# Performance work log

Measured on AMD Instinct MI355X. Metric: run time of the kernel, lower is better.

## Reference

```python
import jax, jax.numpy as jnp
import numpy as np
import math

HEADS = 16
SPH = 64      # size_per_head
KEY = 64      # key_size (defaults to size_per_head)
EMB = 1024
STEP = 3


def extract_seq_patches(x, kernel_size, step):
    # x: [B, L, D] -> [B, L, kernel_size, D]; patch j at pos t is x_pad[t - p_left + j*step]
    B, L, D = x.shape
    k_size = kernel_size + (step - 1) * (kernel_size - 1)
    p_right = (k_size - 1) // 2
    p_left = k_size - 1 - p_right
    xp = jnp.pad(x, ((0, 0), (p_left, p_right), (0, 0)))
    xs = [xp[:, i:i + L] for i in range(0, k_size, step)]  # kernel_size slices
    return jnp.stack(xs, axis=2)


def setup_inputs() -> dict:
    key = jax.random.key(0)
    kx, kq, kk, kv = jax.random.split(key, 4)
    B, L = 2, 4096
    x = jax.random.normal(kx, (B, L, EMB), dtype=jnp.float32)
    W_q = jax.random.normal(kq, (EMB, HEADS * KEY), dtype=jnp.float32) * 0.02
    W_k = jax.random.normal(kk, (EMB, HEADS * KEY), dtype=jnp.float32) * 0.02
    W_v = jax.random.normal(kv, (EMB, HEADS * SPH), dtype=jnp.float32) * 0.02
    return {"x": x, "W_q": W_q, "W_k": W_k, "W_v": W_v}


def _forward(x, W_q, W_k, W_v):
    B, L, D = x.shape
    pad_len = STEP - L % STEP
    x = jnp.pad(x, ((0, 0), (0, pad_len), (0, 0)))
    new_len = L + pad_len
    blocks = new_len // STEP
    q = x @ W_q  # [B, new_len, H*KEY]
    k = x @ W_k
    v = x @ W_v
    ksz = 1 + 2 * (STEP - 1)  # kernel_size = 5
    kp = extract_seq_patches(k, ksz, STEP)  # [B, new_len, ksz, H*KEY]
    vp = extract_seq_patches(v, ksz, STEP)
    # reshape to [B, H, step, blocks, d]
    q = q.reshape(B, blocks, STEP, HEADS, KEY).transpose(0, 3, 2, 1, 4)
    kb = k.reshape(B, blocks, STEP, HEADS, KEY).transpose(0, 3, 2, 1, 4)
    vb = v.reshape(B, blocks, STEP, HEADS, SPH).transpose(0, 3, 2, 1, 4)
    # neighbor patches: [B, H, step, blocks, ksz, d]
    kp = kp.reshape(B, blocks, STEP, ksz, HEADS, KEY).transpose(0, 4, 2, 1, 3, 5)
    vp = vp.reshape(B, blocks, STEP, ksz, HEADS, SPH).transpose(0, 4, 2, 1, 3, 5)
    scale = 1.0 / math.sqrt(KEY)
    # strided attention over blocks (same residue mod step): [B,H,step,blocks,blocks]
    a = jnp.einsum('bhsqk,bhspk->bhsqp', q, kb) * scale
    # block-local neighbor attention: [B,H,step,blocks,ksz]
    ap = jnp.einsum('bhsqk,bhsqnk->bhsqn', q, kp) * scale
    A = jax.nn.softmax(jnp.concatenate([a, ap], axis=-1), axis=-1)
    a, ap = A[..., :blocks], A[..., blocks:]
    o = (jnp.einsum('bhsqp,bhspd->bhsqd', a, vb)
         + jnp.einsum('bhsqn,bhsqnd->bhsqd', ap, vp))
    o = o.transpose(0, 3, 2, 1, 4).reshape(B, new_len, HEADS * SPH)
    return o[:, :L]


def reference(x, W_q, W_k, W_v):
    return _forward(x, W_q, W_k, W_v)
```

## Files before the change

### kernel.cpp

```cpp
#include <hip/hip_runtime.h>
#include <hip/hip_bf16.h>

typedef unsigned int u32;
typedef unsigned short u16;
typedef short s8v __attribute__((ext_vector_type(8)));
typedef short s4v __attribute__((ext_vector_type(4)));
typedef float f4v __attribute__((ext_vector_type(4)));
typedef float f16v __attribute__((ext_vector_type(16)));
typedef u32 u32x2 __attribute__((ext_vector_type(2)));

#define NBLK 1366
#define VROW 1376
#define QSCALE 0.18033688011112042f

__device__ __forceinline__ u16 f2b(float f) {
  u32 u = __builtin_bit_cast(u32, f);
  u = (u + 0x7FFFu + ((u >> 16) & 1u)) >> 16;
  return (u16)u;
}

__device__ __forceinline__ u32 cvtpk(float a, float b) {
  u32 r;
  asm("v_cvt_pk_bf16_f32 %0, %1, %2" : "=v"(r) : "v"(a), "v"(b));
  return r;
}

__device__ __forceinline__ float fexp2(float x) {
#if defined(__has_builtin)
#if __has_builtin(__builtin_amdgcn_exp2f)
  return __builtin_amdgcn_exp2f(x);
#define FEXP2_DONE 1
#endif
#endif
#ifndef FEXP2_DONE
  float r;
  asm("v_exp_f32 %0, %1" : "=v"(r) : "v"(x));
  return r;
#endif
}

__device__ __forceinline__ void gll16(const void* g, void* l) {
  __builtin_amdgcn_global_load_lds(
      (const __attribute__((address_space(1))) u32*)g,
      (__attribute__((address_space(3))) u32*)l, 16, 0, 0);
}

__device__ __forceinline__ f4v mfma32(s8v a, s8v b, f4v c) {
  return __builtin_amdgcn_mfma_f32_16x16x32_bf16(a, b, c, 0, 0, 0);
}

__device__ __forceinline__ f16v mfma3216(s8v a, s8v b, f16v c) {
  return __builtin_amdgcn_mfma_f32_32x32x16_bf16(a, b, c, 0, 0, 0);
}

__device__ __forceinline__ f16v mfma3208(s4v a, s4v b, f16v c) {
#if defined(__has_builtin)
#if __has_builtin(__builtin_amdgcn_mfma_f32_32x32x8bf16_1k)
#define MFMA3208_BUILTIN 1
#endif
#endif
#ifdef MFMA3208_BUILTIN
  return __builtin_amdgcn_mfma_f32_32x32x8bf16_1k(a, b, c, 0, 0, 0);
#else
  f16v d;
  asm("v_mfma_f32_32x32x8_bf16 %0, %1, %2, %3" : "=v"(d) : "v"(a), "v"(b), "v"(c));
  return d;
#endif
}

__device__ __forceinline__ s4v lo4(s8v v) {
  return __builtin_shufflevector(v, v, 0, 1, 2, 3);
}
__device__ __forceinline__ s4v hi4(s8v v) {
  return __builtin_shufflevector(v, v, 4, 5, 6, 7);
}

__global__ __launch_bounds__(256) void k_prep(const float* __restrict__ x,
                                              const float* __restrict__ Wq,
                                              const float* __restrict__ Wk,
                                              const float* __restrict__ Wv,
                                              u16* __restrict__ xb,
                                              u16* __restrict__ Wt,
                                              u16* __restrict__ Vt) {
  const int bid = blockIdx.x;
  const int tid = threadIdx.x;
  if (bid < 4160) {
    long base = ((long)bid * 256 + tid) * 8;
    if (base >= 8320L * 1024L) return;
    int m = (int)(base >> 10);
    int c = (int)(base & 1023);
    int b = m / 4098;
    int t = m - b * 4098;
    s8v pack;
    if (m < 8196 && t < 4096) {
      const float* src = x + ((size_t)b * 4096 + t) * 1024 + c;
      float4 v0 = *(const float4*)(src);
      float4 v1 = *(const float4*)(src + 4);
      pack[0] = (short)f2b(v0.x); pack[1] = (short)f2b(v0.y);
      pack[2] = (short)f2b(v0.z); pack[3] = (short)f2b(v0.w);
      pack[4] = (short)f2b(v1.x); pack[5] = (short)f2b(v1.y);
      pack[6] = (short)f2b(v1.z); pack[7] = (short)f2b(v1.w);
    } else {
#pragma unroll
      for (int i = 0; i < 8; ++i) pack[i] = 0;
    }
    *(s8v*)(xb + base) = pack;
  } else if (bid < 7232) {
    __shared__ float tile[32][33];
    int bid3 = bid - 4160;
    int z = bid3 >> 10;
    int rem = bid3 & 1023;
    const float* W = (z == 0) ? Wq : ((z == 1) ? Wk : Wv);
    u16* dst = Wt + (size_t)z * 1024 * 1024;
    int n0 = (rem & 31) * 32, k0 = (rem >> 5) * 32;
    int tx = tid & 31, ty = tid >> 5;
#pragma unroll
    for (int i = 0; i < 4; ++i)
      tile[ty + i * 8][tx] = W[(size_t)(k0 + ty + i * 8) * 1024 + n0 + tx];
    __syncthreads();
#pragma unroll
    for (int i = 0; i < 4; ++i)
      dst[(size_t)(n0 + ty + i * 8) * 1024 + k0 + tx] = f2b(tile[tx][ty + i * 8]);
  } else {
    int gidx = (bid - 7232) * 256 + tid;
    if (gidx < 6144) {
      u16* dst = Vt + (size_t)gidx * VROW + NBLK;
#pragma unroll
      for (int i = 0; i < 10; ++i) dst[i] = 0;
    } else if (gidx < 6400) {
      Vt[(size_t)6144 * VROW + (gidx - 6144)] = 0;
    }
  }
}

__global__ __launch_bounds__(256) void k_gemm_qkv(const u16* __restrict__ xb,
                                                  const u16* __restrict__ Wt,
                                                  u16* __restrict__ Qp,
                                                  u16* __restrict__ Kp,
                                                  u16* __restrict__ Vt) {
  const int zid = blockIdx.z;
  const int m0 = blockIdx.x * 128;
  const int n0 = blockIdx.y * 128;
  const u16* Bg = Wt + (size_t)zid * 1024 * 1024 + (size_t)n0 * 1024;

  __shared__ __align__(16) u16 shl[16384];
  u16* A0 = shl;
  u16* A1 = shl + 4096;
  u16* B0 = shl + 8192;
  u16* B1 = shl + 12288;

  const int tid = threadIdx.x;
  const int lane = tid & 63;
  const int w = tid >> 6;
  const int wr = w >> 1, wc = w & 1;
  const int lo = lane & 15, g = lane >> 4;

  const int lrow = lane >> 2;
  const int csrc = (lane & 3) ^ ((lane >> 3) & 3);
  const int rsw = (g ^ ((lo >> 1) & 3)) << 4;

  f4v acc[4][4];
#pragma unroll
  for (int i = 0; i < 4; ++i)
#pragma unroll
    for (int j = 0; j < 4; ++j) {
      f4v z = {0.f, 0.f, 0.f, 0.f};
      acc[i][j] = z;
    }

  auto stage = [&](int kt, u16* Ab, u16* Bb) {
#pragma unroll
    for (int c = 0; c < 2; ++c) {
      int rloc = w * 32 + c * 16 + lrow;
      gll16(xb + (size_t)(m0 + rloc) * 1024 + kt + csrc * 8,
            Ab + (w * 32 + c * 16) * 32);
      gll16(Bg + (size_t)rloc * 1024 + kt + csrc * 8,
            Bb + (w * 32 + c * 16) * 32);
    }
  };

  auto compute = [&](const u16* Ab, const u16* Bb) {
    s8v af[4], bf[4];
#pragma unroll
    for (int i = 0; i < 4; ++i) {
      int ar = wr * 64 + i * 16 + lo;
      af[i] = *(const s8v*)((const char*)Ab + ar * 64 + rsw);
      int br = wc * 64 + i * 16 + lo;
      bf[i] = *(const s8v*)((const char*)Bb + br * 64 + rsw);
    }
    __builtin_amdgcn_s_setprio(1);
#pragma unroll
    for (int i = 0; i < 4; ++i)
#pragma unroll
      for (int j = 0; j < 4; ++j)
        acc[i][j] = mfma32(af[i], bf[j], acc[i][j]);
    __builtin_amdgcn_s_setprio(0);
  };

#define BAR_VM4                                             \
  asm volatile("s_waitcnt vmcnt(4)" ::: "memory");          \
  __builtin_amdgcn_s_barrier();                             \
  asm volatile("" ::: "memory");
#define BAR_LGKM                                            \
  asm volatile("s_waitcnt lgkmcnt(0)" ::: "memory");        \
  __builtin_amdgcn_s_barrier();                             \
  asm volatile("" ::: "memory");

  stage(0, A0, B0);
#pragma unroll 1
  for (int kk = 0; kk < 15; ++kk) {
    int kt = kk * 64;
    stage(kt + 32, A1, B1);
    BAR_VM4
    compute(A0, B0);
    BAR_LGKM
    stage(kt + 64, A0, B0);
    BAR_VM4
    compute(A1, B1);
    BAR_LGKM
  }
  stage(31 * 32, A1, B1);
  BAR_VM4
  compute(A0, B0);
  BAR_LGKM
  asm volatile("s_waitcnt vmcnt(0)" ::: "memory");
  __builtin_amdgcn_s_barrier();
  asm volatile("" ::: "memory");
  compute(A1, B1);
  __syncthreads();

#undef BAR_VM4
#undef BAR_LGKM

  const float esc = (zid == 0) ? QSCALE : 1.0f;
  if (zid != 2) {
    u16* dq = (zid == 0) ? Qp : Kp;
#pragma unroll
    for (int i = 0; i < 4; ++i) {
#pragma unroll
      for (int r = 0; r < 4; ++r) {
        int m = m0 + wr * 64 + i * 16 + g * 4 + r;
        if (m >= 8196) continue;
        int b = m / 4098;
        int t = m - b * 4098;
        int s = t % 3;
        int p = t / 3;
        int cb = (b * 3 + s) * 16;
#pragma unroll
        for (int j = 0; j < 4; ++j) {
          int n = n0 + wc * 64 + j * 16 + lo;
          int h = n >> 6, d = n & 63;
          dq[(size_t)((cb + h) * NBLK + p) * 64 + d] = f2b(acc[i][j][r] * esc);
        }
      }
    }
  } else {
    u16* tile = shl;
#pragma unroll
    for (int i = 0; i < 4; ++i)
#pragma unroll
      for (int r = 0; r < 4; ++r) {
        int ml = wr * 64 + i * 16 + g * 4 + r;
#pragma unroll
        for (int j = 0; j < 4; ++j) {
          int nl = wc * 64 + j * 16 + lo;
          tile[ml * 128 + nl] = f2b(acc[i][j][r]);
        }
      }
    __syncthreads();
    for (int pair = tid; pair < 384; pair += 256) {
      int nl = pair & 127;
      int s = pair >> 7;
      int n = n0 + nl;
      int h = n >> 6, d = n & 63;
      for (int b = 0; b < 2; ++b) {
        int mlo = m0 > b * 4098 ? m0 : b * 4098;
        int cap = b * 4098 + 4096;
        int mhi = (m0 + 128 < cap) ? m0 + 128 : cap;
        if (mlo >= mhi) continue;
        int t_lo = mlo - b * 4098;
        int add = (s - (t_lo % 3) + 3) % 3;
        int t = t_lo + add;
        int tend = mhi - b * 4098;
        u16* dst = Vt + (size_t)(((b * 3 + s) * 16 + h) * 64 + d) * VROW;
        for (; t < tend; t += 3)
          dst[t / 3] = tile[(b * 4098 + t - m0) * 128 + nl];
      }
    }
  }
}

__global__ __launch_bounds__(256, 4) void k_attn(const u16* __restrict__ Qp,
                                                 const u16* __restrict__ Kp,
                                                 const u16* __restrict__ Vt,
                                                 float* __restrict__ out) {
  const int wg = blockIdx.x;
  const int idx = (wg & 7) * 132 + (wg >> 3);
  const int combo = idx / 11;
  const int qb = idx - combo * 11;
  const int b = combo / 48;
  const int rem = combo - b * 48;
  const int s = rem >> 4;
  const int h = rem & 15;
  const int tid = threadIdx.x, lane = tid & 63, w = tid >> 6;
  const int lq = lane & 31, lh = lane >> 5;

  const u16* Qg = Qp + (size_t)combo * (NBLK * 64);
  const u16* Kg = Kp + (size_t)combo * (NBLK * 64);
  const u16* Vg = Vt + (size_t)combo * (64 * VROW);

  __shared__ __align__(16) u16 att[2][4][64 * 36];

  const int qg = qb * 128 + w * 32 + lq;
  const int qc = (qg < NBLK) ? qg : (NBLK - 1);
  s8v qf[4];
#pragma unroll
  for (int ss = 0; ss < 4; ++ss)
    qf[ss] = *(const s8v*)(Qg + (size_t)qc * 64 + ss * 16 + lh * 8);

  s4v onesf;
  onesf[0] = onesf[1] = onesf[2] = onesf[3] = (short)0x3F80;

  f16v oacc0, oacc1, den_acc;
#pragma unroll
  for (int i = 0; i < 16; ++i) { oacc0[i] = 0.f; oacc1[i] = 0.f; den_acc[i] = 0.f; }

  const int srow = tid >> 2;
  const int sch = (tid & 3) * 2;
  const int ssub = (tid & 3) * 8;
  s8v kr0, kr1, vr0, vr1;

  auto load_regs = [&](int jt) {
    const int j0 = jt * 64;
    const u16* kp = Kg + (size_t)(j0 + srow) * 64 + sch * 8;
    kr0 = *(const s8v*)(kp);
    kr1 = *(const s8v*)(kp + 8);
    const u16* vp = Vg + (size_t)srow * VROW + j0 + sch * 8;
    vr0 = *(const s8v*)(vp);
    vr1 = *(const s8v*)(vp + 8);
  };

  auto stage_write = [&](int slot) {
    u16* K0 = att[slot][0];
    u16* K1 = att[slot][1];
    u16* V0 = att[slot][2];
    u16* V1 = att[slot][3];
    const int kb = srow * 36 + ssub;
    *(s4v*)(K0 + kb) = lo4(kr0);
    *(s4v*)(K0 + kb + 4) = hi4(kr0);
    *(s4v*)(K1 + kb) = lo4(kr1);
    *(s4v*)(K1 + kb + 4) = hi4(kr1);
    const int vb0 = srow * 36 + sch * 4;
    *(s4v*)(V0 + vb0) = lo4(vr0);
    *(s4v*)(V1 + vb0) = hi4(vr0);
    *(s4v*)(V0 + vb0 + 4) = lo4(vr1);
    *(s4v*)(V1 + vb0 + 4) = hi4(vr1);
  };

  const int qmin = qb * 128;

  auto compute = [&](int slot, int jt) {
    const int j0 = jt * 64;
    const u16* Kb = att[slot][lh];
    const u16* Vb0 = att[slot][2];
    const u16* Vb1 = att[slot][3];
    const u16* Vme = (lh == 0) ? Vb0 : Vb1;

    const bool special = ((j0 <= qmin + 130) && (j0 + 65 >= qmin)) || (j0 + 64 > NBLK);
    s4v ef[8];
#pragma unroll
    for (int jb = 0; jb < 2; ++jb) {
      f16v sacc;
#pragma unroll
      for (int i = 0; i < 16; ++i) sacc[i] = 0.f;
      __builtin_amdgcn_s_setprio(1);
#pragma unroll
      for (int ss = 0; ss < 4; ++ss) {
        const u16* kp = Kb + (jb * 32 + lq) * 36 + ss * 8;
        s4v a = *(const s4v*)kp;
        s4v b2 = *(const s4v*)(kp + 4);
        s8v kf = __builtin_shufflevector(a, b2, 0, 1, 2, 3, 4, 5, 6, 7);
        sacc = mfma3216(kf, qf[ss], sacc);
      }
      __builtin_amdgcn_s_setprio(0);

      if (special) {
        float e[16];
#pragma unroll
        for (int r = 0; r < 16; ++r) {
          int j = j0 + jb * 32 + (r & 3) + 8 * (r >> 2) + 4 * lh;
          float ev = fexp2(sacc[r]);
          int dd = j - qg;
          float fac = (j < NBLK) ? (((dd <= 2) && (dd >= -2)) ? 2.f : 1.f) : 0.f;
          e[r] = ev * fac;
        }
#pragma unroll
        for (int k4 = 0; k4 < 4; ++k4) {
          u32x2 w2;
          w2[0] = cvtpk(e[k4 * 4 + 0], e[k4 * 4 + 1]);
          w2[1] = cvtpk(e[k4 * 4 + 2], e[k4 * 4 + 3]);
          ef[jb * 4 + k4] = __builtin_bit_cast(s4v, w2);
        }
      } else {
#pragma unroll
        for (int k4 = 0; k4 < 4; ++k4) {
          u32x2 w2;
          w2[0] = cvtpk(fexp2(sacc[k4 * 4 + 0]), fexp2(sacc[k4 * 4 + 1]));
          w2[1] = cvtpk(fexp2(sacc[k4 * 4 + 2]), fexp2(sacc[k4 * 4 + 3]));
          ef[jb * 4 + k4] = __builtin_bit_cast(s4v, w2);
        }
      }
    }

    __builtin_amdgcn_s_setprio(1);
#pragma unroll
    for (int ks = 0; ks < 8; ++ks)
      den_acc = mfma3208(ef[ks], onesf, den_acc);
#pragma unroll
    for (int ks = 0; ks < 8; ++ks) {
      s4v vf0 = *(const s4v*)(Vme + lq * 36 + ks * 4);
      s4v vf1 = *(const s4v*)(Vme + (32 + lq) * 36 + ks * 4);
      oacc0 = mfma3208(ef[ks], vf0, oacc0);
      oacc1 = mfma3208(ef[ks], vf1, oacc1);
    }
    __builtin_amdgcn_s_setprio(0);
  };

#define LGKM_BAR                                            \
  asm volatile("s_waitcnt lgkmcnt(0)" ::: "memory");        \
  __builtin_amdgcn_s_barrier();                             \
  asm volatile("" ::: "memory");

  load_regs(0);
  stage_write(0);
  load_regs(1);
  LGKM_BAR

#pragma unroll 1
  for (int t = 0; t < 21; ++t) {
    compute(t & 1, t);
    stage_write((t + 1) & 1);
    if (t < 20) load_regs(t + 2);
    LGKM_BAR
  }
  compute(1, 21);

#undef LGKM_BAR

  const int hbase = h * 64;
#pragma unroll
  for (int r = 0; r < 16; ++r) {
    int q = qb * 128 + w * 32 + (r & 3) + 8 * (r >> 2) + 4 * lh;
    float dden = den_acc[r];
    dden += (q == 0 || q == NBLK - 1) ? 2.f : ((q == 1 || q == NBLK - 2) ? 1.f : 0.f);
    float rr = 1.f / dden;
    int t = 3 * q + s;
    if (q < NBLK && t < 4096) {
      float* orow = out + ((size_t)b * 4096 + t) * 1024 + hbase + lq;
      orow[0] = oacc0[r] * rr;
      orow[32] = oacc1[r] * rr;
    }
  }
}

extern "C" void kernel_launch(void* const* d_in, const int* in_sizes, int n_in,
                              void* d_out, int out_size, void* d_ws, size_t ws_size,
                              hipStream_t stream) {
  const float* x  = (const float*)d_in[0];
  const float* Wq = (const float*)d_in[1];
  const float* Wk = (const float*)d_in[2];
  const float* Wv = (const float*)d_in[3];
  float* out = (float*)d_out;

  u16* ws = (u16*)d_ws;
  u16* xb = ws;
  u16* Wt = xb + 8519680;
  u16* Qp = Wt + 3145728;
  u16* Kp = Qp + 8392704;
  u16* Vt = Kp + 8392704;

  k_prep<<<dim3(7257), 256, 0, stream>>>(x, Wq, Wk, Wv, xb, Wt, Vt);
  k_gemm_qkv<<<dim3(65, 8, 3), 256, 0, stream>>>(xb, Wt, Qp, Kp, Vt);
  k_attn<<<dim3(1056), 256, 0, stream>>>(Qp, Kp, Vt, out);
}
```

Baseline: 217.6 us.

## Use 32x32x16 MFMA for PV via permlane32 swap, compute denominator with VALU sums

```diff
diff --git a/kernel.cpp b/kernel.cpp
--- a/kernel.cpp
+++ b/kernel.cpp
@@ -8,6 +8,7 @@
 typedef float f4v __attribute__((ext_vector_type(4)));
 typedef float f16v __attribute__((ext_vector_type(16)));
 typedef u32 u32x2 __attribute__((ext_vector_type(2)));
+typedef u32 u32x4 __attribute__((ext_vector_type(4)));
 
 #define NBLK 1366
 #define VROW 1376
@@ -51,21 +52,6 @@
 
 __device__ __forceinline__ f16v mfma3216(s8v a, s8v b, f16v c) {
   return __builtin_amdgcn_mfma_f32_32x32x16_bf16(a, b, c, 0, 0, 0);
-}
-
-__device__ __forceinline__ f16v mfma3208(s4v a, s4v b, f16v c) {
-#if defined(__has_builtin)
-#if __has_builtin(__builtin_amdgcn_mfma_f32_32x32x8bf16_1k)
-#define MFMA3208_BUILTIN 1
-#endif
-#endif
-#ifdef MFMA3208_BUILTIN
-  return __builtin_amdgcn_mfma_f32_32x32x8bf16_1k(a, b, c, 0, 0, 0);
-#else
-  f16v d;
-  asm("v_mfma_f32_32x32x8_bf16 %0, %1, %2, %3" : "=v"(d) : "v"(a), "v"(b), "v"(c));
-  return d;
-#endif
 }
 
 __device__ __forceinline__ s4v lo4(s8v v) {
@@ -318,12 +304,10 @@
   for (int ss = 0; ss < 4; ++ss)
     qf[ss] = *(const s8v*)(Qg + (size_t)qc * 64 + ss * 16 + lh * 8);
 
-  s4v onesf;
-  onesf[0] = onesf[1] = onesf[2] = onesf[3] = (short)0x3F80;
-
-  f16v oacc0, oacc1, den_acc;
-#pragma unroll
-  for (int i = 0; i < 16; ++i) { oacc0[i] = 0.f; oacc1[i] = 0.f; den_acc[i] = 0.f; }
+  f16v oacc0, oacc1;
+#pragma unroll
+  for (int i = 0; i < 16; ++i) { oacc0[i] = 0.f; oacc1[i] = 0.f; }
+  float dpart[4] = {0.f, 0.f, 0.f, 0.f};
 
   const int srow = tid >> 2;
   const int sch = (tid & 3) * 2;
@@ -362,12 +346,10 @@
   auto compute = [&](int slot, int jt) {
     const int j0 = jt * 64;
     const u16* Kb = att[slot][lh];
-    const u16* Vb0 = att[slot][2];
-    const u16* Vb1 = att[slot][3];
-    const u16* Vme = (lh == 0) ? Vb0 : Vb1;
+    const u16* Vl0 = att[slot][2];
+    const u16* Vl1 = att[slot][3];
 
     const bool special = ((j0 <= qmin + 130) && (j0 + 65 >= qmin)) || (j0 + 64 > NBLK);
-    s4v ef[8];
 #pragma unroll
     for (int jb = 0; jb < 2; ++jb) {
       f16v sacc;
@@ -384,8 +366,8 @@
       }
       __builtin_amdgcn_s_setprio(0);
 
+      float e[16];
       if (special) {
-        float e[16];
 #pragma unroll
         for (int r = 0; r < 16; ++r) {
           int j = j0 + jb * 32 + (r & 3) + 8 * (r >> 2) + 4 * lh;
@@ -394,36 +376,37 @@
           float fac = (j < NBLK) ? (((dd <= 2) && (dd >= -2)) ? 2.f : 1.f) : 0.f;
           e[r] = ev * fac;
         }
-#pragma unroll
-        for (int k4 = 0; k4 < 4; ++k4) {
-          u32x2 w2;
-          w2[0] = cvtpk(e[k4 * 4 + 0], e[k4 * 4 + 1]);
-          w2[1] = cvtpk(e[k4 * 4 + 2], e[k4 * 4 + 3]);
-          ef[jb * 4 + k4] = __builtin_bit_cast(s4v, w2);
-        }
       } else {
 #pragma unroll
-        for (int k4 = 0; k4 < 4; ++k4) {
-          u32x2 w2;
-          w2[0] = cvtpk(fexp2(sacc[k4 * 4 + 0]), fexp2(sacc[k4 * 4 + 1]));
-          w2[1] = cvtpk(fexp2(sacc[k4 * 4 + 2]), fexp2(sacc[k4 * 4 + 3]));
-          ef[jb * 4 + k4] = __builtin_bit_cast(s4v, w2);
-        }
-      }
-    }
-
-    __builtin_amdgcn_s_setprio(1);
-#pragma unroll
-    for (int ks = 0; ks < 8; ++ks)
-      den_acc = mfma3208(ef[ks], onesf, den_acc);
-#pragma unroll
-    for (int ks = 0; ks < 8; ++ks) {
-      s4v vf0 = *(const s4v*)(Vme + lq * 36 + ks * 4);
-      s4v vf1 = *(const s4v*)(Vme + (32 + lq) * 36 + ks * 4);
-      oacc0 = mfma3208(ef[ks], vf0, oacc0);
-      oacc1 = mfma3208(ef[ks], vf1, oacc1);
-    }
-    __builtin_amdgcn_s_setprio(0);
+        for (int r = 0; r < 16; ++r) e[r] = fexp2(sacc[r]);
+      }
+#pragma unroll
+      for (int r = 0; r < 16; ++r) dpart[r & 3] += e[r];
+
+#pragma unroll
+      for (int g2 = 0; g2 < 2; ++g2) {
+        u32 pe0 = cvtpk(e[g2 * 8 + 0], e[g2 * 8 + 1]);
+        u32 pe1 = cvtpk(e[g2 * 8 + 2], e[g2 * 8 + 3]);
+        u32 pe2 = cvtpk(e[g2 * 8 + 4], e[g2 * 8 + 5]);
+        u32 pe3 = cvtpk(e[g2 * 8 + 6], e[g2 * 8 + 7]);
+        asm("v_permlane32_swap_b32 %0, %1" : "+v"(pe0), "+v"(pe2));
+        asm("v_permlane32_swap_b32 %0, %1" : "+v"(pe1), "+v"(pe3));
+        u32x4 fw;
+        fw[0] = pe0; fw[1] = pe1; fw[2] = pe2; fw[3] = pe3;
+        s8v ef8 = __builtin_bit_cast(s8v, fw);
+        const int ci = (jb * 4 + g2 * 2 + lh) * 4;
+        s4v v0a = *(const s4v*)(Vl0 + lq * 36 + ci);
+        s4v v0b = *(const s4v*)(Vl1 + lq * 36 + ci);
+        s8v vf0 = __builtin_shufflevector(v0a, v0b, 0, 1, 2, 3, 4, 5, 6, 7);
+        s4v v1a = *(const s4v*)(Vl0 + (32 + lq) * 36 + ci);
+        s4v v1b = *(const s4v*)(Vl1 + (32 + lq) * 36 + ci);
+        s8v vf1 = __builtin_shufflevector(v1a, v1b, 0, 1, 2, 3, 4, 5, 6, 7);
+        __builtin_amdgcn_s_setprio(1);
+        oacc0 = mfma3216(ef8, vf0, oacc0);
+        oacc1 = mfma3216(ef8, vf1, oacc1);
+        __builtin_amdgcn_s_setprio(0);
+      }
+    }
   };
 
 #define LGKM_BAR                                            \
@@ -447,13 +430,17 @@
 
 #undef LGKM_BAR
 
+  float dtot = (dpart[0] + dpart[1]) + (dpart[2] + dpart[3]);
+  dtot += __shfl_xor(dtot, 32, 64);
+
   const int hbase = h * 64;
 #pragma unroll
   for (int r = 0; r < 16; ++r) {
-    int q = qb * 128 + w * 32 + (r & 3) + 8 * (r >> 2) + 4 * lh;
-    float dden = den_acc[r];
-    dden += (q == 0 || q == NBLK - 1) ? 2.f : ((q == 1 || q == NBLK - 2) ? 1.f : 0.f);
-    float rr = 1.f / dden;
+    int cr = (r & 3) + 8 * (r >> 2) + 4 * lh;
+    int q = qb * 128 + w * 32 + cr;
+    float dq = __shfl(dtot, cr, 64);
+    dq += (q == 0 || q == NBLK - 1) ? 2.f : ((q == 1 || q == NBLK - 2) ? 1.f : 0.f);
+    float rr = 1.f / dq;
     int t = 3 * q + s;
     if (q < NBLK && t < 4096) {
       float* orow = out + ((size_t)b * 4096 + t) * 1024 + hbase + lq;
```

Result: faster. 207.9 us (-4.5%).
